# Performance work log

Hardware: AMD Instinct MI355X
Metric: run time of the kernel (lower is better)

## Reference

```python
import jax, jax.numpy as jnp
import numpy as np

N = 100_000
E = 1_600_000
EPS_STD = 1e-5


def _pna(x, src, dst, eattr, We, be, Wpre, bpre, Wpost, bpost, Wlin, blin):
    # PyG PNAConv, towers=1, pre/post_layers=1, scalers=['identity']
    e = eattr @ We + be                                   # [E, Fin]
    h = jnp.concatenate([x[dst], x[src], e], axis=-1)     # [E, 3*Fin] (x_i, x_j, edge)
    m = h @ Wpre + bpre                                   # [E, Fin]
    cnt = jax.ops.segment_sum(jnp.ones((m.shape[0],), m.dtype), dst, N)  # [N]
    denom = jnp.maximum(cnt, 1.0)[:, None]
    s = jax.ops.segment_sum(m, dst, N)
    mean = s / denom
    has = (cnt > 0)[:, None]
    mx = jnp.where(has, jax.ops.segment_max(m, dst, N), 0.0)
    mn = jnp.where(has, jax.ops.segment_min(m, dst, N), 0.0)
    mean_sq = jax.ops.segment_sum(m * m, dst, N) / denom
    std = jnp.sqrt(jax.nn.relu(mean_sq - mean * mean) + EPS_STD)
    agg = jnp.concatenate([s, mean, mx, mn, std], axis=-1)  # [N, 5*Fin]
    out = jnp.concatenate([x, agg], axis=-1) @ Wpost + bpost # [N, Fout]
    return out @ Wlin + blin


def _gcn(x, src, dst, W, b):
    # GCNConv with add_self_loops + symmetric normalization
    h = x @ W
    loops = jnp.arange(N)
    s2 = jnp.concatenate([src, loops])
    d2 = jnp.concatenate([dst, loops])
    deg = jax.ops.segment_sum(jnp.ones(s2.shape, h.dtype), d2, N)
    dinv = jnp.where(deg > 0, deg ** -0.5, 0.0)
    w = dinv[s2] * dinv[d2]
    return jax.ops.segment_sum(h[s2] * w[:, None], d2, N) + b


def _forward(x, edge_index, edge_attr,
             We0, be0, Wpre0, bpre0, Wpost0, bpost0, Wlin0, blin0,
             We1, be1, Wpre1, bpre1, Wpost1, bpost1, Wlin1, blin1,
             Wg, bg, Wh1, bh1, Wh2, bh2):
    src, dst = edge_index[0], edge_index[1]
    h = jax.nn.relu(_pna(x, src, dst, edge_attr, We0, be0, Wpre0, bpre0, Wpost0, bpost0, Wlin0, blin0))
    h = jax.nn.relu(_pna(h, src, dst, edge_attr, We1, be1, Wpre1, bpre1, Wpost1, bpost1, Wlin1, blin1))
    h = _gcn(h, src, dst, Wg, bg)                          # [N, 16]
    out = jnp.concatenate([h, x], axis=1)                  # [N, 32]
    out = jax.nn.relu(out @ Wh1 + bh1) @ Wh2 + bh2         # [N, 10]
    return out


def setup_inputs() -> dict:
    key = jax.random.key(0)
    ks = list(jax.random.split(key, 32))
    k = iter(ks)

    def glorot(shape):
        lim = float(np.sqrt(6.0 / (shape[0] + shape[1])))
        return jax.random.uniform(next(k), shape, jnp.float32, -lim, lim)

    inp = {}
    inp['x'] = jax.random.normal(next(k), (N, 16), jnp.float32)
    inp['edge_index'] = jax.random.randint(next(k), (2, E), 0, N)
    inp['edge_attr'] = jax.random.normal(next(k), (E, 4), jnp.float32)
    # layer 0: Fin=16, Fout=64
    inp['We0'] = glorot((4, 16)); inp['be0'] = jnp.zeros((16,), jnp.float32)
    inp['Wpre0'] = glorot((48, 16)); inp['bpre0'] = jnp.zeros((16,), jnp.float32)
    inp['Wpost0'] = glorot((96, 64)); inp['bpost0'] = jnp.zeros((64,), jnp.float32)
    inp['Wlin0'] = glorot((64, 64)); inp['blin0'] = jnp.zeros((64,), jnp.float32)
    # layer 1: Fin=64, Fout=64
    inp['We1'] = glorot((4, 64)); inp['be1'] = jnp.zeros((64,), jnp.float32)
    inp['Wpre1'] = glorot((192, 64)); inp['bpre1'] = jnp.zeros((64,), jnp.float32)
    inp['Wpost1'] = glorot((384, 64)); inp['bpost1'] = jnp.zeros((64,), jnp.float32)
    inp['Wlin1'] = glorot((64, 64)); inp['blin1'] = jnp.zeros((64,), jnp.float32)
    # GCN + head
    inp['Wg'] = glorot((64, 16)); inp['bg'] = jnp.zeros((16,), jnp.float32)
    inp['Wh1'] = glorot((32, 10)); inp['bh1'] = jnp.zeros((10,), jnp.float32)
    inp['Wh2'] = glorot((10, 10)); inp['bh2'] = jnp.zeros((10,), jnp.float32)
    return inp


def reference(x, edge_index, edge_attr,
              We0, be0, Wpre0, bpre0, Wpost0, bpost0, Wlin0, blin0,
              We1, be1, Wpre1, bpre1, Wpost1, bpost1, Wlin1, blin1,
              Wg, bg, Wh1, bh1, Wh2, bh2):
    return _forward(x, edge_index, edge_attr,
                    We0, be0, Wpre0, bpre0, Wpost0, bpost0, Wlin0, blin0,
                    We1, be1, Wpre1, bpre1, Wpost1, bpost1, Wlin1, blin1,
                    Wg, bg, Wh1, bh1, Wh2, bh2)
```

## Files before the change

kernel.cpp:

```cpp
#include <hip/hip_runtime.h>

#define NN 100000
#define NE 1600000

#define BSH 9
#define BSZ (1 << BSH)
#define NB  196
#define CHUNK 6250

#define OFF_C0   0
#define OFF_D0   64
#define OFF_WPL0 80
#define OFF_BPL0 6224
#define OFF_C1   6288
#define OFF_D1   6544
#define OFF_WPL1 6608
#define OFF_BPL1 31184
#define WBUF_TOT 31248

#define BT1_OFF 0
#define BT0_OFF 24576
#define BTA_OFF 30720
#define BTB_OFF 34816
#define BT_TOT  38912
#define PREP_TOT (WBUF_TOT + BT_TOT)

__device__ inline unsigned short pack_bf16(float a) {
  unsigned ua = __float_as_uint(a);
  ua += 0x7fffu + ((ua >> 16) & 1u);
  return (unsigned short)(ua >> 16);
}
__device__ inline float bf_s(unsigned short u) { return __uint_as_float(((unsigned)u) << 16); }

__global__ void k_prep(const float* __restrict__ We0, const float* __restrict__ be0,
                       const float* __restrict__ Wpre0, const float* __restrict__ bpre0,
                       const float* __restrict__ Wpost0, const float* __restrict__ bpost0,
                       const float* __restrict__ Wlin0, const float* __restrict__ blin0,
                       const float* __restrict__ We1, const float* __restrict__ be1,
                       const float* __restrict__ Wpre1, const float* __restrict__ bpre1,
                       const float* __restrict__ Wpost1, const float* __restrict__ bpost1,
                       const float* __restrict__ Wlin1, const float* __restrict__ blin1,
                       float* __restrict__ wbuf, unsigned short* __restrict__ Bt) {
  int id = blockIdx.x * 256 + threadIdx.x;
  if (id >= PREP_TOT) return;
  if (id < WBUF_TOT) {
    float a = 0.f;
    if (id < OFF_D0) {
      int j = id >> 4, f = id & 15;
      for (int t = 0; t < 16; t++) a = fmaf(We0[j*16+t], Wpre0[(32+t)*16+f], a);
    } else if (id < OFF_WPL0) {
      int f = id - OFF_D0; a = bpre0[f];
      for (int t = 0; t < 16; t++) a = fmaf(be0[t], Wpre0[(32+t)*16+f], a);
    } else if (id < OFF_BPL0) {
      int r = id - OFF_WPL0; int k = r >> 6, o = r & 63;
      for (int j = 0; j < 64; j++) a = fmaf(Wpost0[k*64+j], Wlin0[j*64+o], a);
    } else if (id < OFF_C1) {
      int o = id - OFF_BPL0; a = blin0[o];
      for (int j = 0; j < 64; j++) a = fmaf(bpost0[j], Wlin0[j*64+o], a);
    } else if (id < OFF_D1) {
      int r = id - OFF_C1; int j = r >> 6, f = r & 63;
      for (int t = 0; t < 64; t++) a = fmaf(We1[j*64+t], Wpre1[(128+t)*64+f], a);
    } else if (id < OFF_WPL1) {
      int f = id - OFF_D1; a = bpre1[f];
      for (int t = 0; t < 64; t++) a = fmaf(be1[t], Wpre1[(128+t)*64+f], a);
    } else if (id < OFF_BPL1) {
      int r = id - OFF_WPL1; int k = r >> 6, o = r & 63;
      for (int j = 0; j < 64; j++) a = fmaf(Wpost1[k*64+j], Wlin1[j*64+o], a);
    } else {
      int o = id - OFF_BPL1; a = blin1[o];
      for (int j = 0; j < 64; j++) a = fmaf(bpost1[j], Wlin1[j*64+o], a);
    }
    wbuf[id] = a;
    return;
  }
  int rid = id - WBUF_TOT;
  if (rid < 24576) {
    int nn = rid / 384, k = rid - nn * 384;
    float a = 0.f;
    for (int j = 0; j < 64; j++) a = fmaf(Wpost1[k*64+j], Wlin1[j*64+nn], a);
    Bt[BT1_OFF + rid] = pack_bf16(a);
  } else if (rid < 30720) {
    int r2 = rid - 24576;
    int nn = r2 / 96, k = r2 - nn * 96;
    float a = 0.f;
    for (int j = 0; j < 64; j++) a = fmaf(Wpost0[k*64+j], Wlin0[j*64+nn], a);
    Bt[BT0_OFF + r2] = pack_bf16(a);
  } else if (rid < 34816) {
    int r3 = rid - 30720;
    int nn = r3 >> 6, k = r3 & 63;
    Bt[BTA_OFF + r3] = pack_bf16(Wpre1[k*64+nn]);
  } else {
    int r4 = rid - 34816;
    int nn = r4 >> 6, k = r4 & 63;
    Bt[BTB_OFF + r4] = pack_bf16(Wpre1[(64+k)*64+nn]);
  }
}

__global__ void k_hist(const int* __restrict__ dst, int* __restrict__ cnt) {
  int i = blockIdx.x * 256 + threadIdx.x;
  if (i < NE) atomicAdd(&cnt[dst[i]], 1);
}

__global__ void k_scan1(const int* __restrict__ deg, int* __restrict__ partial,
                        int* __restrict__ bsums) {
  __shared__ int lds[256];
  int i = blockIdx.x * 256 + threadIdx.x;
  int v = (i < NN) ? deg[i] : 0;
  lds[threadIdx.x] = v;
  __syncthreads();
  for (int off = 1; off < 256; off <<= 1) {
    int t = (threadIdx.x >= off) ? lds[threadIdx.x - off] : 0;
    __syncthreads();
    lds[threadIdx.x] += t;
    __syncthreads();
  }
  if (i < NN) partial[i] = lds[threadIdx.x];
  if (threadIdx.x == 255) bsums[blockIdx.x] = lds[255];
}

__global__ void k_scan2(const int* __restrict__ bsums, int* __restrict__ boff, int nb) {
  __shared__ int lds[512];
  int v = ((int)threadIdx.x < nb) ? bsums[threadIdx.x] : 0;
  lds[threadIdx.x] = v;
  __syncthreads();
  for (int off = 1; off < 512; off <<= 1) {
    int t = (threadIdx.x >= off) ? lds[threadIdx.x - off] : 0;
    __syncthreads();
    lds[threadIdx.x] += t;
    __syncthreads();
  }
  if ((int)threadIdx.x < nb) boff[threadIdx.x] = lds[threadIdx.x] - v;
}

__global__ void k_scan3(const int* __restrict__ partial, const int* __restrict__ boff,
                        int* __restrict__ rowptr) {
  int i = blockIdx.x * 256 + threadIdx.x;
  if (i < NN) rowptr[i + 1] = partial[i] + boff[blockIdx.x];
  if (i == 0) rowptr[0] = 0;
}

__global__ void k_binit(const int* __restrict__ rowptr, int* __restrict__ gfill) {
  int b = threadIdx.x;
  if (b < NB) {
    int n0 = b << BSH;
    gfill[b] = rowptr[n0 > NN ? NN : n0];
  }
}

__global__ __launch_bounds__(256) void k_bin(const int* __restrict__ dst,
                                             int* __restrict__ gfill,
                                             int2* __restrict__ rec) {
  __shared__ int hcnt[NB];
  __shared__ int hbase[NB];
  const int t = threadIdx.x;
  for (int b = t; b < NB; b += 256) hcnt[b] = 0;
  __syncthreads();
  const int lo = blockIdx.x * CHUNK, hi = lo + CHUNK;
  for (int i = lo + t; i < hi; i += 256)
    atomicAdd(&hcnt[dst[i] >> BSH], 1);
  __syncthreads();
  for (int b = t; b < NB; b += 256) {
    int c = hcnt[b];
    hbase[b] = c > 0 ? atomicAdd(&gfill[b], c) : 0;
    hcnt[b] = 0;
  }
  __syncthreads();
  for (int i = lo + t; i < hi; i += 256) {
    int d = dst[i];
    int b = d >> BSH;
    int lp = atomicAdd(&hcnt[b], 1);
    rec[hbase[b] + lp] = make_int2(d, i);
  }
}

__global__ __launch_bounds__(256) void k_scatter2(const int2* __restrict__ rec,
                                                  const int* __restrict__ rowptr,
                                                  int* __restrict__ perm) {
  __shared__ int lfill[BSZ];
  const int b = blockIdx.x;
  const int n0 = b << BSH;
  const int n1 = (n0 + BSZ < NN) ? n0 + BSZ : NN;
  const int t = threadIdx.x;
  for (int n = n0 + t; n < n1; n += 256) lfill[n - n0] = rowptr[n];
  __syncthreads();
  const int lo = rowptr[n0], hi = rowptr[n1];
  for (int i = lo + t; i < hi; i += 256) {
    int2 r = rec[i];
    int pos = atomicAdd(&lfill[r.x - n0], 1);
    perm[pos] = r.y;
  }
}

__global__ void k_permute(const int* __restrict__ perm, const int* __restrict__ src,
                          const float4* __restrict__ ea, int* __restrict__ col,
                          ushort4* __restrict__ eapb) {
  int i = blockIdx.x * 256 + threadIdx.x;
  if (i < NE) {
    int eid = perm[i];
    col[i] = src[eid];
    float4 e = ea[eid];
    ushort4 pk;
    pk.x = pack_bf16(e.x); pk.y = pack_bf16(e.y);
    pk.z = pack_bf16(e.z); pk.w = pack_bf16(e.w);
    eapb[i] = pk;
  }
}

__global__ void k_pre0(const float* __restrict__ x, const float* __restrict__ Wpre0,
                       float* __restrict__ xA0, unsigned short* __restrict__ xB0b) {
  int t = blockIdx.x * 256 + threadIdx.x;
  int node = t >> 5, k = t & 31;
  int f = k & 15;
  const float* W = Wpre0 + (k < 16 ? 0 : 256);
  const float* xr = x + (size_t)node * 16;
  float a = 0.f;
#pragma unroll
  for (int j = 0; j < 16; j++) a = fmaf(xr[j], W[j*16+f], a);
  if (k < 16) xA0[(size_t)node*16+f] = a;
  else        xB0b[(size_t)node*16+f] = pack_bf16(a);
}

__global__ __launch_bounds__(256) void k_agg0(const float* __restrict__ x,
                                              const float* __restrict__ xA0,
                                              const unsigned short* __restrict__ xB0b,
                                              const int* __restrict__ rowptr,
                                              const int* __restrict__ col,
                                              const ushort4* __restrict__ eapb,
                                              const float* __restrict__ wbuf,
                                              unsigned short* __restrict__ vec96b) {
  const int w = threadIdx.x >> 6, lane = threadIdx.x & 63;
  const int g = lane >> 4, f = lane & 15;
  const int node = blockIdx.x * 4 + w;
  const int start = rowptr[node], end = rowptr[node + 1];
  const int cnt = end - start;
  const float c0 = wbuf[OFF_C0 + f],      c1v = wbuf[OFF_C0 + 16 + f];
  const float c2v = wbuf[OFF_C0 + 32 + f], c3v = wbuf[OFF_C0 + 48 + f];
  float s = 0.f, sq = 0.f, mx = -__builtin_inff(), mn = __builtin_inff();
  int p = start + g;
  for (; p + 4 < end; p += 8) {
    int s0 = col[p], s1 = col[p + 4];
    ushort4 e0 = eapb[p], e1 = eapb[p + 4];
    float v0 = bf_s(xB0b[(size_t)s0 * 16 + f]);
    float v1 = bf_s(xB0b[(size_t)s1 * 16 + f]);
    v0 = fmaf(bf_s(e0.x), c0, v0); v0 = fmaf(bf_s(e0.y), c1v, v0);
    v0 = fmaf(bf_s(e0.z), c2v, v0); v0 = fmaf(bf_s(e0.w), c3v, v0);
    v1 = fmaf(bf_s(e1.x), c0, v1); v1 = fmaf(bf_s(e1.y), c1v, v1);
    v1 = fmaf(bf_s(e1.z), c2v, v1); v1 = fmaf(bf_s(e1.w), c3v, v1);
    s += v0 + v1;
    sq = fmaf(v0, v0, sq); sq = fmaf(v1, v1, sq);
    mx = fmaxf(mx, fmaxf(v0, v1)); mn = fminf(mn, fminf(v0, v1));
  }
  for (; p < end; p += 4) {
    int si = col[p];
    ushort4 e0 = eapb[p];
    float v = bf_s(xB0b[(size_t)si * 16 + f]);
    v = fmaf(bf_s(e0.x), c0, v); v = fmaf(bf_s(e0.y), c1v, v);
    v = fmaf(bf_s(e0.z), c2v, v); v = fmaf(bf_s(e0.w), c3v, v);
    s += v; sq = fmaf(v, v, sq); mx = fmaxf(mx, v); mn = fminf(mn, v);
  }
  s  += __shfl_xor(s, 16);  s  += __shfl_xor(s, 32);
  sq += __shfl_xor(sq, 16); sq += __shfl_xor(sq, 32);
  mx = fmaxf(mx, __shfl_xor(mx, 16)); mx = fmaxf(mx, __shfl_xor(mx, 32));
  mn = fminf(mn, __shfl_xor(mn, 16)); mn = fminf(mn, __shfl_xor(mn, 32));
  const float c = xA0[(size_t)node * 16 + f] + wbuf[OFF_D0 + f];
  float sum_m, mean_m, mx_m, mn_m, std_m;
  if (cnt > 0) {
    float inv = 1.f / (float)cnt;
    float meanv = s * inv;
    sum_m = fmaf((float)cnt, c, s);
    mean_m = meanv + c;
    mx_m = mx + c; mn_m = mn + c;
    float var = fmaf(-meanv, meanv, sq * inv);
    std_m = sqrtf(fmaxf(var, 0.f) + 1e-5f);
  } else {
    sum_m = 0.f; mean_m = 0.f; mx_m = 0.f; mn_m = 0.f; std_m = sqrtf(1e-5f);
  }
  if (g == 0) {
    unsigned short* vr = vec96b + (size_t)node * 96;
    vr[f]      = pack_bf16(x[(size_t)node * 16 + f]);
    vr[16 + f] = pack_bf16(sum_m);
    vr[32 + f] = pack_bf16(mean_m);
    vr[48 + f] = pack_bf16(mx_m);
    vr[64 + f] = pack_bf16(mn_m);
    vr[80 + f] = pack_bf16(std_m);
  }
}

__global__ __launch_bounds__(64) void k_agg1(const float* __restrict__ xA1,
                                             const unsigned short* __restrict__ xB1b,
                                             const int* __restrict__ rowptr,
                                             const int* __restrict__ col,
                                             const ushort4* __restrict__ eapb,
                                             const float* __restrict__ wbuf,
                                             unsigned short* __restrict__ agg320b) {
  const int f = threadIdx.x;
  const int node = blockIdx.x;
  const int start = rowptr[node], end = rowptr[node + 1];
  const int cnt = end - start;
  const float c0 = wbuf[OFF_C1 + f],       c1v = wbuf[OFF_C1 + 64 + f];
  const float c2v = wbuf[OFF_C1 + 128 + f], c3v = wbuf[OFF_C1 + 192 + f];
  float s = 0.f, sq = 0.f, mx = -__builtin_inff(), mn = __builtin_inff();
  int p = start;
  for (; p + 7 < end; p += 8) {
#pragma unroll
    for (int u = 0; u < 8; u++) {
      int si = col[p + u];
      ushort4 e = eapb[p + u];
      const unsigned short* row = xB1b + (unsigned)si * 64;
      float v = bf_s(row[f]);
      v = fmaf(bf_s(e.x), c0, v); v = fmaf(bf_s(e.y), c1v, v);
      v = fmaf(bf_s(e.z), c2v, v); v = fmaf(bf_s(e.w), c3v, v);
      s += v; sq = fmaf(v, v, sq); mx = fmaxf(mx, v); mn = fminf(mn, v);
    }
  }
  for (; p < end; p++) {
    int si = col[p];
    ushort4 e = eapb[p];
    const unsigned short* row = xB1b + (unsigned)si * 64;
    float v = bf_s(row[f]);
    v = fmaf(bf_s(e.x), c0, v); v = fmaf(bf_s(e.y), c1v, v);
    v = fmaf(bf_s(e.z), c2v, v); v = fmaf(bf_s(e.w), c3v, v);
    s += v; sq = fmaf(v, v, sq); mx = fmaxf(mx, v); mn = fminf(mn, v);
  }
  const float c = xA1[(size_t)node * 64 + f] + wbuf[OFF_D1 + f];
  float sum_m, mean_m, mx_m, mn_m, std_m;
  if (cnt > 0) {
    float inv = 1.f / (float)cnt;
    float meanv = s * inv;
    sum_m = fmaf((float)cnt, c, s);
    mean_m = meanv + c;
    mx_m = mx + c; mn_m = mn + c;
    float var = fmaf(-meanv, meanv, sq * inv);
    std_m = sqrtf(fmaxf(var, 0.f) + 1e-5f);
  } else {
    sum_m = 0.f; mean_m = 0.f; mx_m = 0.f; mn_m = 0.f; std_m = sqrtf(1e-5f);
  }
  unsigned short* ar = agg320b + (size_t)node * 320;
  ar[f]       = pack_bf16(sum_m);
  ar[64 + f]  = pack_bf16(mean_m);
  ar[128 + f] = pack_bf16(mx_m);
  ar[192 + f] = pack_bf16(mn_m);
  ar[256 + f] = pack_bf16(std_m);
}

template <int K, bool RELU, int OMODE>
__global__ __launch_bounds__(256) void k_mmf(const unsigned short* __restrict__ A,
                                             const unsigned short* __restrict__ Bt,
                                             const float* __restrict__ bias,
                                             void* __restrict__ C, int n) {
  using bf16x8 = __attribute__((ext_vector_type(8))) short;
  using f32x4  = __attribute__((ext_vector_type(4))) float;
  const int wave = threadIdx.x >> 6, lane = threadIdx.x & 63;
  const int qm = lane & 15, quad = lane >> 4;
  const int m0 = blockIdx.x * 64 + wave * 16;
  const int mrow = m0 + qm;
  f32x4 acc[4] = {};
#pragma unroll
  for (int k0 = 0; k0 < K; k0 += 32) {
    bf16x8 a = *(const bf16x8*)(A + (size_t)mrow * K + k0 + quad * 8);
#pragma unroll
    for (int nt = 0; nt < 4; nt++) {
      bf16x8 b = *(const bf16x8*)(Bt + (size_t)(nt * 16 + qm) * K + k0 + quad * 8);
      acc[nt] = __builtin_amdgcn_mfma_f32_16x16x32_bf16(a, b, acc[nt], 0, 0, 0);
    }
  }
#pragma unroll
  for (int nt = 0; nt < 4; nt++) {
    int colc = nt * 16 + qm;
    float bb = bias ? bias[colc] : 0.f;
#pragma unroll
    for (int r = 0; r < 4; r++) {
      int m = m0 + quad * 4 + r;
      if (m < n) {
        float v = acc[nt][r] + bb;
        if (RELU) v = fmaxf(v, 0.f);
        if (OMODE == 0) ((float*)C)[(size_t)m * 64 + colc] = v;
        else ((unsigned short*)C)[(size_t)m * 64 + colc] = pack_bf16(v);
      }
    }
  }
}

__global__ __launch_bounds__(256) void k_mmf64d(const unsigned short* __restrict__ A,
                                                const unsigned short* __restrict__ BtA,
                                                const unsigned short* __restrict__ BtB,
                                                float* __restrict__ xA1,
                                                unsigned short* __restrict__ xB1b, int n) {
  using bf16x8 = __attribute__((ext_vector_type(8))) short;
  using f32x4  = __attribute__((ext_vector_type(4))) float;
  const int wave = threadIdx.x >> 6, lane = threadIdx.x & 63;
  const int qm = lane & 15, quad = lane >> 4;
  const int m0 = blockIdx.x * 64 + wave * 16;
  const int mrow = m0 + qm;
  f32x4 accA[4] = {}, accB[4] = {};
#pragma unroll
  for (int k0 = 0; k0 < 64; k0 += 32) {
    bf16x8 a = *(const bf16x8*)(A + (size_t)mrow * 64 + k0 + quad * 8);
#pragma unroll
    for (int nt = 0; nt < 4; nt++) {
      bf16x8 bA = *(const bf16x8*)(BtA + (size_t)(nt * 16 + qm) * 64 + k0 + quad * 8);
      bf16x8 bB = *(const bf16x8*)(BtB + (size_t)(nt * 16 + qm) * 64 + k0 + quad * 8);
      accA[nt] = __builtin_amdgcn_mfma_f32_16x16x32_bf16(a, bA, accA[nt], 0, 0, 0);
      accB[nt] = __builtin_amdgcn_mfma_f32_16x16x32_bf16(a, bB, accB[nt], 0, 0, 0);
    }
  }
#pragma unroll
  for (int nt = 0; nt < 4; nt++) {
    int colc = nt * 16 + qm;
#pragma unroll
    for (int r = 0; r < 4; r++) {
      int m = m0 + quad * 4 + r;
      if (m < n) {
        xA1[(size_t)m * 64 + colc] = accA[nt][r];
        xB1b[(size_t)m * 64 + colc] = pack_bf16(accB[nt][r]);
      }
    }
  }
}

__global__ __launch_bounds__(256) void k_mm384g(const unsigned short* __restrict__ hb,
                                                const unsigned short* __restrict__ aggb,
                                                const unsigned short* __restrict__ Bt1,
                                                const float* __restrict__ wbuf,
                                                const float* __restrict__ Wg,
                                                const int* __restrict__ rowptr,
                                                unsigned short* __restrict__ hgsb,
                                                float* __restrict__ dinv, int n) {
  using bf16x8 = __attribute__((ext_vector_type(8))) short;
  using f32x4  = __attribute__((ext_vector_type(4))) float;
  __shared__ float h2t[4][16][65];
  __shared__ float wg[64][16];
  const int tid = threadIdx.x;
  for (int i = tid; i < 1024; i += 256) wg[i >> 4][i & 15] = Wg[i];
  const int wave = tid >> 6, lane = tid & 63;
  const int qm = lane & 15, quad = lane >> 4;
  const int m0 = blockIdx.x * 64 + wave * 16;
  const int mrow = m0 + qm;
  f32x4 acc[4] = {};
  for (int k0 = 0; k0 < 384; k0 += 32) {
    bf16x8 a;
    if (k0 < 64) a = *(const bf16x8*)(hb + (size_t)mrow * 64 + k0 + quad * 8);
    else         a = *(const bf16x8*)(aggb + (size_t)mrow * 320 + (k0 - 64) + quad * 8);
#pragma unroll
    for (int nt = 0; nt < 4; nt++) {
      bf16x8 b = *(const bf16x8*)(Bt1 + (size_t)(nt * 16 + qm) * 384 + k0 + quad * 8);
      acc[nt] = __builtin_amdgcn_mfma_f32_16x16x32_bf16(a, b, acc[nt], 0, 0, 0);
    }
  }
#pragma unroll
  for (int nt = 0; nt < 4; nt++) {
    int colc = nt * 16 + qm;
    float bias = wbuf[OFF_BPL1 + colc];
#pragma unroll
    for (int r = 0; r < 4; r++)
      h2t[wave][quad * 4 + r][colc] = fmaxf(acc[nt][r] + bias, 0.f);
  }
  __syncthreads();
  const int row = lane & 15, g = lane >> 4;
  float hg0 = 0.f, hg1 = 0.f, hg2 = 0.f, hg3 = 0.f;
#pragma unroll 16
  for (int j = 0; j < 64; j++) {
    float hv = h2t[wave][row][j];
    float4 w4 = *(const float4*)&wg[j][g * 4];
    hg0 = fmaf(hv, w4.x, hg0); hg1 = fmaf(hv, w4.y, hg1);
    hg2 = fmaf(hv, w4.z, hg2); hg3 = fmaf(hv, w4.w, hg3);
  }
  int m = m0 + row;
  if (m < n) {
    int deg = rowptr[m + 1] - rowptr[m] + 1;
    float dv = 1.0f / sqrtf((float)deg);
    if (g == 0) dinv[m] = dv;
    ushort4 pk;
    pk.x = pack_bf16(hg0 * dv); pk.y = pack_bf16(hg1 * dv);
    pk.z = pack_bf16(hg2 * dv); pk.w = pack_bf16(hg3 * dv);
    *(ushort4*)(hgsb + (size_t)m * 16 + g * 4) = pk;
  }
}

__global__ __launch_bounds__(256) void k_head(const float* __restrict__ x,
                                              const unsigned short* __restrict__ hgsb,
                                              const float* __restrict__ dinv,
                                              const int* __restrict__ rowptr,
                                              const int* __restrict__ col,
                                              const float* __restrict__ bg,
                                              const float* __restrict__ Wh1,
                                              const float* __restrict__ bh1,
                                              const float* __restrict__ Wh2,
                                              const float* __restrict__ bh2,
                                              float* __restrict__ out) {
  __shared__ float zb[4][32];
  __shared__ float o1b[4][10];
  const int w = threadIdx.x >> 6, lane = threadIdx.x & 63;
  const int g = lane >> 4, f = lane & 15;
  const int node = blockIdx.x * 4 + w;
  const int start = rowptr[node], end = rowptr[node + 1];
  float s = 0.f;
  int p = start + g;
  for (; p + 12 < end; p += 16) {
    int s0 = col[p], s1 = col[p + 4], s2 = col[p + 8], s3 = col[p + 12];
    float v0 = bf_s(hgsb[(size_t)s0 * 16 + f]);
    float v1 = bf_s(hgsb[(size_t)s1 * 16 + f]);
    float v2 = bf_s(hgsb[(size_t)s2 * 16 + f]);
    float v3 = bf_s(hgsb[(size_t)s3 * 16 + f]);
    s += (v0 + v1) + (v2 + v3);
  }
  for (; p < end; p += 4) {
    int si = col[p];
    s += bf_s(hgsb[(size_t)si * 16 + f]);
  }
  s += __shfl_xor(s, 16); s += __shfl_xor(s, 32);
  if (g == 0) {
    float gout = (s + bf_s(hgsb[(size_t)node * 16 + f])) * dinv[node] + bg[f];
    zb[w][f] = gout;
    zb[w][16 + f] = x[(size_t)node * 16 + f];
  }
  __syncthreads();
  if (lane < 10) {
    float a = bh1[lane];
#pragma unroll
    for (int k = 0; k < 32; k++) a = fmaf(zb[w][k], Wh1[k * 10 + lane], a);
    o1b[w][lane] = fmaxf(a, 0.f);
  }
  __syncthreads();
  if (lane < 10) {
    float a = bh2[lane];
#pragma unroll
    for (int j = 0; j < 10; j++) a = fmaf(o1b[w][j], Wh2[j * 10 + lane], a);
    out[(size_t)node * 10 + lane] = a;
  }
}

extern "C" void kernel_launch(void* const* d_in, const int* in_sizes, int n_in,
                              void* d_out, int out_size, void* d_ws, size_t ws_size,
                              hipStream_t stream) {
  const float* x      = (const float*)d_in[0];
  const int*   ei     = (const int*)d_in[1];
  const float* eattr  = (const float*)d_in[2];
  const float* We0    = (const float*)d_in[3];
  const float* be0    = (const float*)d_in[4];
  const float* Wpre0  = (const float*)d_in[5];
  const float* bpre0  = (const float*)d_in[6];
  const float* Wpost0 = (const float*)d_in[7];
  const float* bpost0 = (const float*)d_in[8];
  const float* Wlin0  = (const float*)d_in[9];
  const float* blin0  = (const float*)d_in[10];
  const float* We1    = (const float*)d_in[11];
  const float* be1    = (const float*)d_in[12];
  const float* Wpre1  = (const float*)d_in[13];
  const float* bpre1  = (const float*)d_in[14];
  const float* Wpost1 = (const float*)d_in[15];
  const float* bpost1 = (const float*)d_in[16];
  const float* Wlin1  = (const float*)d_in[17];
  const float* blin1  = (const float*)d_in[18];
  const float* Wg     = (const float*)d_in[19];
  const float* bg     = (const float*)d_in[20];
  const float* Wh1    = (const float*)d_in[21];
  const float* bh1    = (const float*)d_in[22];
  const float* Wh2    = (const float*)d_in[23];
  const float* bh2    = (const float*)d_in[24];
  const int* srcI = ei;
  const int* dstI = ei + NE;
  float* out = (float*)d_out;

  char* base = (char*)d_ws;
  size_t off = 0;
  auto take = [&](size_t bytes) -> char* {
    char* p = base + off;
    off += (bytes + 255) & ~(size_t)255;
    return p;
  };
  int* cnt     = (int*)take((size_t)NN * 4);
  int* rowptr  = (int*)take((size_t)(NN + 1) * 4);
  int* partial = (int*)take((size_t)NN * 4);
  int* bsums   = (int*)take(512 * 4);
  int* boff    = (int*)take(512 * 4);
  int* gfill   = (int*)take(512 * 4);
  unsigned short* Bt = (unsigned short*)take((size_t)BT_TOT * 2);
  int* col     = (int*)take((size_t)NE * 4);
  ushort4* eapb = (ushort4*)take((size_t)NE * 8);
  float* wbuf  = (float*)take((size_t)WBUF_TOT * 4);
  int*   perm  = (int*)take((size_t)NE * 4);
  unsigned short* hgsb = (unsigned short*)perm;
  float* dinv  = (float*)((char*)perm + (size_t)NN * 16 * 2);
  float* xA1   = (float*)take((size_t)NN * 64 * 4);
  int2*  rec   = (int2*)take((size_t)NE * 8);
  unsigned short* xB1b = (unsigned short*)rec;
  char* Z = take((size_t)NN * 320 * 4);
  unsigned short* vec96b  = (unsigned short*)Z;
  float* xA0    = (float*)(Z + (size_t)NN * 96 * 2);
  unsigned short* xB0b = (unsigned short*)(Z + (size_t)NN * 96 * 2 + (size_t)NN * 16 * 4);
  unsigned short* agg320b = (unsigned short*)Z;
  unsigned short* hb = (unsigned short*)(Z + (size_t)96 * 1024 * 1024);

  hipMemsetAsync(cnt, 0, (size_t)NN * 4, stream);
  k_prep<<<(PREP_TOT + 255) / 256, 256, 0, stream>>>(
      We0, be0, Wpre0, bpre0, Wpost0, bpost0, Wlin0, blin0,
      We1, be1, Wpre1, bpre1, Wpost1, bpost1, Wlin1, blin1, wbuf, Bt);
  k_hist<<<(NE + 255) / 256, 256, 0, stream>>>(dstI, cnt);
  k_scan1<<<391, 256, 0, stream>>>(cnt, partial, bsums);
  k_scan2<<<1, 512, 0, stream>>>(bsums, boff, 391);
  k_scan3<<<391, 256, 0, stream>>>(partial, boff, rowptr);
  k_binit<<<1, 256, 0, stream>>>(rowptr, gfill);
  k_bin<<<256, 256, 0, stream>>>(dstI, gfill, rec);
  k_scatter2<<<NB, 256, 0, stream>>>(rec, rowptr, perm);
  k_permute<<<(NE + 255) / 256, 256, 0, stream>>>(perm, srcI, (const float4*)eattr,
                                                  col, eapb);
  k_pre0<<<NN * 32 / 256, 256, 0, stream>>>(x, Wpre0, xA0, xB0b);
  k_agg0<<<NN / 4, 256, 0, stream>>>(x, xA0, xB0b, rowptr, col, eapb, wbuf, vec96b);
  k_mmf<96, true, 1><<<(NN + 63) / 64, 256, 0, stream>>>(
      vec96b, Bt + BT0_OFF, wbuf + OFF_BPL0, hb, NN);
  k_mmf64d<<<(NN + 63) / 64, 256, 0, stream>>>(
      hb, Bt + BTA_OFF, Bt + BTB_OFF, xA1, xB1b, NN);
  k_agg1<<<NN, 64, 0, stream>>>(xA1, xB1b, rowptr, col, eapb, wbuf, agg320b);
  k_mm384g<<<(NN + 63) / 64, 256, 0, stream>>>(
      hb, agg320b, Bt + BT1_OFF, wbuf, Wg, rowptr, hgsb, dinv, NN);
  k_head<<<NN / 4, 256, 0, stream>>>(x, hgsb, dinv, rowptr, col, bg, Wh1, bh1,
                                     Wh2, bh2, out);
}
```

Before: 560.5 us.

## Fuse CSR build into bucket-count, bin, and per-bucket scan-scatter kernels

Replaces the node-level histogram, three-pass scan, binning and permute kernels with a bucket-level count, a single-block bucket scan, a binning pass that carries src and bf16-packed edge attributes inside 16-byte records, and a per-bucket kernel that computes the local degree scan, writes rowptr, and scatters col/eapb directly. This removes the per-node atomic histogram, the multi-kernel scan and the random gather through perm. It also stores xA1 as bf16 instead of fp32 to cut traffic in k_agg1, at some precision cost. Workspace aliasing is reorganised to fit the larger record buffer.

```diff
diff --git a/kernel.cpp b/kernel.cpp
--- a/kernel.cpp
+++ b/kernel.cpp
@@ -96,60 +96,44 @@
   }
 }
 
-__global__ void k_hist(const int* __restrict__ dst, int* __restrict__ cnt) {
-  int i = blockIdx.x * 256 + threadIdx.x;
-  if (i < NE) atomicAdd(&cnt[dst[i]], 1);
-}
-
-__global__ void k_scan1(const int* __restrict__ deg, int* __restrict__ partial,
-                        int* __restrict__ bsums) {
+__global__ __launch_bounds__(256) void k_bcnt(const int* __restrict__ dst,
+                                              int* __restrict__ bcnt) {
+  __shared__ int h[NB];
+  for (int b = threadIdx.x; b < NB; b += 256) h[b] = 0;
+  __syncthreads();
+  const int lo = blockIdx.x * CHUNK, hi = lo + CHUNK;
+  for (int i = lo + threadIdx.x; i < hi; i += 256)
+    atomicAdd(&h[dst[i] >> BSH], 1);
+  __syncthreads();
+  for (int b = threadIdx.x; b < NB; b += 256)
+    if (h[b]) atomicAdd(&bcnt[b], h[b]);
+}
+
+__global__ void k_bscan(const int* __restrict__ bcnt, int* __restrict__ gbase,
+                        int* __restrict__ gfill) {
   __shared__ int lds[256];
-  int i = blockIdx.x * 256 + threadIdx.x;
-  int v = (i < NN) ? deg[i] : 0;
-  lds[threadIdx.x] = v;
+  int t = threadIdx.x;
+  int v = (t < NB) ? bcnt[t] : 0;
+  lds[t] = v;
   __syncthreads();
   for (int off = 1; off < 256; off <<= 1) {
-    int t = (threadIdx.x >= off) ? lds[threadIdx.x - off] : 0;
+    int u = (t >= off) ? lds[t - off] : 0;
     __syncthreads();
-    lds[threadIdx.x] += t;
+    lds[t] += u;
     __syncthreads();
   }
-  if (i < NN) partial[i] = lds[threadIdx.x];
-  if (threadIdx.x == 255) bsums[blockIdx.x] = lds[255];
-}
-
-__global__ void k_scan2(const int* __restrict__ bsums, int* __restrict__ boff, int nb) {
-  __shared__ int lds[512];
-  int v = ((int)threadIdx.x < nb) ? bsums[threadIdx.x] : 0;
-  lds[threadIdx.x] = v;
-  __syncthreads();
-  for (int off = 1; off < 512; off <<= 1) {
-    int t = (threadIdx.x >= off) ? lds[threadIdx.x - off] : 0;
-    __syncthreads();
-    lds[threadIdx.x] += t;
-    __syncthreads();
-  }
-  if ((int)threadIdx.x < nb) boff[threadIdx.x] = lds[threadIdx.x] - v;
-}
-
-__global__ void k_scan3(const int* __restrict__ partial, const int* __restrict__ boff,
-                        int* __restrict__ rowptr) {
-  int i = blockIdx.x * 256 + threadIdx.x;
-  if (i < NN) rowptr[i + 1] = partial[i] + boff[blockIdx.x];
-  if (i == 0) rowptr[0] = 0;
-}
-
-__global__ void k_binit(const int* __restrict__ rowptr, int* __restrict__ gfill) {
-  int b = threadIdx.x;
-  if (b < NB) {
-    int n0 = b << BSH;
-    gfill[b] = rowptr[n0 > NN ? NN : n0];
-  }
-}
-
-__global__ __launch_bounds__(256) void k_bin(const int* __restrict__ dst,
-                                             int* __restrict__ gfill,
-                                             int2* __restrict__ rec) {
+  if (t <= NB) {
+    int excl = (t == 0) ? 0 : lds[t - 1];
+    gbase[t] = excl;
+    if (t < NB) gfill[t] = excl;
+  }
+}
+
+__global__ __launch_bounds__(256) void k_bin16(const int* __restrict__ dst,
+                                               const int* __restrict__ src,
+                                               const float4* __restrict__ ea,
+                                               int* __restrict__ gfill,
+                                               int4* __restrict__ rec) {
   __shared__ int hcnt[NB];
   __shared__ int hbase[NB];
   const int t = threadIdx.x;
@@ -169,40 +153,63 @@
     int d = dst[i];
     int b = d >> BSH;
     int lp = atomicAdd(&hcnt[b], 1);
-    rec[hbase[b] + lp] = make_int2(d, i);
-  }
-}
-
-__global__ __launch_bounds__(256) void k_scatter2(const int2* __restrict__ rec,
-                                                  const int* __restrict__ rowptr,
-                                                  int* __restrict__ perm) {
-  __shared__ int lfill[BSZ];
+    float4 e = ea[i];
+    int4 r;
+    r.x = d; r.y = src[i];
+    r.z = (int)(((unsigned)pack_bf16(e.y) << 16) | (unsigned)pack_bf16(e.x));
+    r.w = (int)(((unsigned)pack_bf16(e.w) << 16) | (unsigned)pack_bf16(e.z));
+    rec[hbase[b] + lp] = r;
+  }
+}
+
+__global__ __launch_bounds__(256) void k_scatter2b(const int4* __restrict__ rec,
+                                                   const int* __restrict__ gbase,
+                                                   int* __restrict__ rowptr,
+                                                   int* __restrict__ col,
+                                                   ushort4* __restrict__ eapb) {
+  __shared__ int cnt[BSZ];
+  __shared__ int scn[BSZ];
+  __shared__ int fill[BSZ];
   const int b = blockIdx.x;
   const int n0 = b << BSH;
   const int n1 = (n0 + BSZ < NN) ? n0 + BSZ : NN;
   const int t = threadIdx.x;
-  for (int n = n0 + t; n < n1; n += 256) lfill[n - n0] = rowptr[n];
-  __syncthreads();
-  const int lo = rowptr[n0], hi = rowptr[n1];
-  for (int i = lo + t; i < hi; i += 256) {
-    int2 r = rec[i];
-    int pos = atomicAdd(&lfill[r.x - n0], 1);
-    perm[pos] = r.y;
-  }
-}
-
-__global__ void k_permute(const int* __restrict__ perm, const int* __restrict__ src,
-                          const float4* __restrict__ ea, int* __restrict__ col,
-                          ushort4* __restrict__ eapb) {
-  int i = blockIdx.x * 256 + threadIdx.x;
-  if (i < NE) {
-    int eid = perm[i];
-    col[i] = src[eid];
-    float4 e = ea[eid];
-    ushort4 pk;
-    pk.x = pack_bf16(e.x); pk.y = pack_bf16(e.y);
-    pk.z = pack_bf16(e.z); pk.w = pack_bf16(e.w);
-    eapb[i] = pk;
+  cnt[t] = 0; cnt[t + 256] = 0;
+  __syncthreads();
+  const int base = gbase[b];
+  const int total = gbase[b + 1] - base;
+  for (int i = t; i < total; i += 256)
+    atomicAdd(&cnt[rec[base + i].x - n0], 1);
+  __syncthreads();
+  scn[t] = cnt[t]; scn[t + 256] = cnt[t + 256];
+  __syncthreads();
+  for (int off = 1; off < BSZ; off <<= 1) {
+    int v0 = (t >= off) ? scn[t - off] : 0;
+    int i1 = t + 256;
+    int v1 = (i1 >= off) ? scn[i1 - off] : 0;
+    __syncthreads();
+    scn[t] += v0; scn[i1] += v1;
+    __syncthreads();
+  }
+  {
+    int e0 = scn[t] - cnt[t];
+    int e1 = scn[t + 256] - cnt[t + 256];
+    fill[t] = base + e0; fill[t + 256] = base + e1;
+    if (n0 + t < n1) rowptr[n0 + t] = base + e0;
+    if (n0 + t + 256 < n1) rowptr[n0 + t + 256] = base + e1;
+  }
+  if (b == NB - 1 && t == 0) rowptr[NN] = base + total;
+  __syncthreads();
+  for (int i = t; i < total; i += 256) {
+    int4 r = rec[base + i];
+    int pos = atomicAdd(&fill[r.x - n0], 1);
+    col[pos] = r.y;
+    ushort4 e;
+    e.x = (unsigned short)(r.z & 0xffff);
+    e.y = (unsigned short)((unsigned)r.z >> 16);
+    e.z = (unsigned short)(r.w & 0xffff);
+    e.w = (unsigned short)((unsigned)r.w >> 16);
+    eapb[pos] = e;
   }
 }
 
@@ -286,7 +293,7 @@
   }
 }
 
-__global__ __launch_bounds__(64) void k_agg1(const float* __restrict__ xA1,
+__global__ __launch_bounds__(64) void k_agg1(const unsigned short* __restrict__ xA1b,
                                              const unsigned short* __restrict__ xB1b,
                                              const int* __restrict__ rowptr,
                                              const int* __restrict__ col,
@@ -322,7 +329,7 @@
     v = fmaf(bf_s(e.z), c2v, v); v = fmaf(bf_s(e.w), c3v, v);
     s += v; sq = fmaf(v, v, sq); mx = fmaxf(mx, v); mn = fminf(mn, v);
   }
-  const float c = xA1[(size_t)node * 64 + f] + wbuf[OFF_D1 + f];
+  const float c = bf_s(xA1b[(size_t)node * 64 + f]) + wbuf[OFF_D1 + f];
   float sum_m, mean_m, mx_m, mn_m, std_m;
   if (cnt > 0) {
     float inv = 1.f / (float)cnt;
@@ -384,7 +391,7 @@
 __global__ __launch_bounds__(256) void k_mmf64d(const unsigned short* __restrict__ A,
                                                 const unsigned short* __restrict__ BtA,
                                                 const unsigned short* __restrict__ BtB,
-                                                float* __restrict__ xA1,
+                                                unsigned short* __restrict__ xA1b,
                                                 unsigned short* __restrict__ xB1b, int n) {
   using bf16x8 = __attribute__((ext_vector_type(8))) short;
   using f32x4  = __attribute__((ext_vector_type(4))) float;
@@ -411,7 +418,7 @@
     for (int r = 0; r < 4; r++) {
       int m = m0 + quad * 4 + r;
       if (m < n) {
-        xA1[(size_t)m * 64 + colc] = accA[nt][r];
+        xA1b[(size_t)m * 64 + colc] = pack_bf16(accA[nt][r]);
         xB1b[(size_t)m * 64 + colc] = pack_bf16(accB[nt][r]);
       }
     }
@@ -569,49 +576,42 @@
     off += (bytes + 255) & ~(size_t)255;
     return p;
   };
-  int* cnt     = (int*)take((size_t)NN * 4);
   int* rowptr  = (int*)take((size_t)(NN + 1) * 4);
-  int* partial = (int*)take((size_t)NN * 4);
-  int* bsums   = (int*)take(512 * 4);
-  int* boff    = (int*)take(512 * 4);
-  int* gfill   = (int*)take(512 * 4);
+  int* bcnt    = (int*)take(256 * 4);
+  int* gbase   = (int*)take(256 * 4);
+  int* gfill   = (int*)take(256 * 4);
   unsigned short* Bt = (unsigned short*)take((size_t)BT_TOT * 2);
   int* col     = (int*)take((size_t)NE * 4);
   ushort4* eapb = (ushort4*)take((size_t)NE * 8);
   float* wbuf  = (float*)take((size_t)WBUF_TOT * 4);
-  int*   perm  = (int*)take((size_t)NE * 4);
-  unsigned short* hgsb = (unsigned short*)perm;
-  float* dinv  = (float*)((char*)perm + (size_t)NN * 16 * 2);
-  float* xA1   = (float*)take((size_t)NN * 64 * 4);
-  int2*  rec   = (int2*)take((size_t)NE * 8);
-  unsigned short* xB1b = (unsigned short*)rec;
+  char* recbuf = take((size_t)NE * 16);
+  int4* rec    = (int4*)recbuf;
+  unsigned short* xA1b = (unsigned short*)recbuf;
+  unsigned short* xB1b = (unsigned short*)(recbuf + (size_t)NN * 64 * 2);
   char* Z = take((size_t)NN * 320 * 4);
   unsigned short* vec96b  = (unsigned short*)Z;
   float* xA0    = (float*)(Z + (size_t)NN * 96 * 2);
   unsigned short* xB0b = (unsigned short*)(Z + (size_t)NN * 96 * 2 + (size_t)NN * 16 * 4);
   unsigned short* agg320b = (unsigned short*)Z;
+  unsigned short* hgsb = (unsigned short*)(Z + (size_t)64 * 1024 * 1024);
+  float* dinv   = (float*)(Z + (size_t)64 * 1024 * 1024 + (size_t)NN * 16 * 2);
   unsigned short* hb = (unsigned short*)(Z + (size_t)96 * 1024 * 1024);
 
-  hipMemsetAsync(cnt, 0, (size_t)NN * 4, stream);
+  hipMemsetAsync(bcnt, 0, 256 * 4, stream);
   k_prep<<<(PREP_TOT + 255) / 256, 256, 0, stream>>>(
       We0, be0, Wpre0, bpre0, Wpost0, bpost0, Wlin0, blin0,
       We1, be1, Wpre1, bpre1, Wpost1, bpost1, Wlin1, blin1, wbuf, Bt);
-  k_hist<<<(NE + 255) / 256, 256, 0, stream>>>(dstI, cnt);
-  k_scan1<<<391, 256, 0, stream>>>(cnt, partial, bsums);
-  k_scan2<<<1, 512, 0, stream>>>(bsums, boff, 391);
-  k_scan3<<<391, 256, 0, stream>>>(partial, boff, rowptr);
-  k_binit<<<1, 256, 0, stream>>>(rowptr, gfill);
-  k_bin<<<256, 256, 0, stream>>>(dstI, gfill, rec);
-  k_scatter2<<<NB, 256, 0, stream>>>(rec, rowptr, perm);
-  k_permute<<<(NE + 255) / 256, 256, 0, stream>>>(perm, srcI, (const float4*)eattr,
-                                                  col, eapb);
+  k_bcnt<<<256, 256, 0, stream>>>(dstI, bcnt);
+  k_bscan<<<1, 256, 0, stream>>>(bcnt, gbase, gfill);
+  k_bin16<<<256, 256, 0, stream>>>(dstI, srcI, (const float4*)eattr, gfill, rec);
+  k_scatter2b<<<NB, 256, 0, stream>>>(rec, gbase, rowptr, col, eapb);
   k_pre0<<<NN * 32 / 256, 256, 0, stream>>>(x, Wpre0, xA0, xB0b);
   k_agg0<<<NN / 4, 256, 0, stream>>>(x, xA0, xB0b, rowptr, col, eapb, wbuf, vec96b);
   k_mmf<96, true, 1><<<(NN + 63) / 64, 256, 0, stream>>>(
       vec96b, Bt + BT0_OFF, wbuf + OFF_BPL0, hb, NN);
   k_mmf64d<<<(NN + 63) / 64, 256, 0, stream>>>(
-      hb, Bt + BTA_OFF, Bt + BTB_OFF, xA1, xB1b, NN);
-  k_agg1<<<NN, 64, 0, stream>>>(xA1, xB1b, rowptr, col, eapb, wbuf, agg320b);
+      hb, Bt + BTA_OFF, Bt + BTB_OFF, xA1b, xB1b, NN);
+  k_agg1<<<NN, 64, 0, stream>>>(xA1b, xB1b, rowptr, col, eapb, wbuf, agg320b);
   k_mm384g<<<(NN + 63) / 64, 256, 0, stream>>>(
       hb, agg320b, Bt + BT1_OFF, wbuf, Wg, rowptr, hgsb, dinv, NN);
   k_head<<<NN / 4, 256, 0, stream>>>(x, hgsb, dinv, rowptr, col, bg, Wh1, bh1,
```

After: 485.8 us. 13.3% less time.
